# Optimization experiments

Measured on AMD Instinct MI355X. Metric: run time of the kernel, lower is better.

Reference implementation:

```python
import jax, jax.numpy as jnp
import numpy as np

C = 256      # embed_dim
GROUP = 2    # conv groups
K = 3        # kernel/pool size
K2 = K * K
OG = 8       # offset groups (hard-coded in Similarity_cal)
NEX = 3      # exemplars per image (out_conv expects group*3*4 channels)


def conv2d(x, w, b, pad):
    y = jax.lax.conv_general_dilated(x, w, (1, 1), [(pad, pad), (pad, pad)],
                                     dimension_numbers=("NCHW", "OIHW", "NCHW"))
    return y + b[None, :, None, None]


def ln_c(x, g, b, eps=1e-5):
    # LayerNorm over the channel axis of NCHW (torch permutes to NHWC, LN, permute back)
    mu = x.mean(axis=1, keepdims=True)
    var = ((x - mu) ** 2).mean(axis=1, keepdims=True)
    return (x - mu) / jnp.sqrt(var + eps) * g[None, :, None, None] + b[None, :, None, None]


def bilinear_gather(img, py, px):
    # img [Cg,H,W]; py,px [K2,H,W] -> samples [Cg,K2,H,W], zero outside borders
    Cg, H, W = img.shape
    y0f = jnp.floor(py); x0f = jnp.floor(px)
    wy = py - y0f; wx = px - x0f
    y0 = y0f.astype(jnp.int32); x0 = x0f.astype(jnp.int32)
    flat = img.reshape(Cg, H * W)

    def corner(yy, xx, w):
        valid = (yy >= 0) & (yy < H) & (xx >= 0) & (xx < W)
        idx = jnp.clip(yy, 0, H - 1) * W + jnp.clip(xx, 0, W - 1)
        v = jnp.take(flat, idx.reshape(-1), axis=1).reshape(Cg, K2, H, W)
        return v * (w * valid)[None]

    return (corner(y0, x0, (1 - wy) * (1 - wx)) + corner(y0, x0 + 1, (1 - wy) * wx)
            + corner(y0 + 1, x0, wy * (1 - wx)) + corner(y0 + 1, x0 + 1, wy * wx))


def deform_conv(x, offset, mask, weight, dilation):
    # x [C,H,W]; offset [2*OG*K2,H,W]; mask [OG*K2,H,W] (softmaxed); weight [NEX*GROUP, C//GROUP, K, K]
    Cc, H, W = x.shape
    pad = (K - 1) * dilation // 2
    off = offset.reshape(OG, K2, 2, H, W)  # (dy, dx) per offset-group / tap
    kk = jnp.arange(K, dtype=x.dtype)
    ky = jnp.repeat(kk, K) * dilation - pad  # [K2]
    kx = jnp.tile(kk, K) * dilation - pad
    ii = jnp.arange(H, dtype=x.dtype)
    jj = jnp.arange(W, dtype=x.dtype)
    py = ii[None, None, :, None] + ky[None, :, None, None] + off[:, :, 0]  # [OG,K2,H,W]
    px = jj[None, None, None, :] + kx[None, :, None, None] + off[:, :, 1]
    xg = x.reshape(OG, Cc // OG, H, W)
    samp = jax.vmap(bilinear_gather)(xg, py, px)              # [OG,Cg,K2,H,W]
    samp = samp * mask.reshape(OG, 1, K2, H, W)               # modulation
    samp = samp.reshape(GROUP, Cc // GROUP, K2, H, W)
    wR = weight.reshape(NEX * GROUP, Cc // GROUP, K2)
    gidx = jnp.arange(NEX * GROUP) // NEX                     # out-channel -> conv group
    return jnp.einsum("rck,rckhw->rhw", wR, samp[gidx])       # [NEX*GROUP,H,W]


def forward(querys_feat, supports_feat, in_w, in_b, ln_g, ln_b, out_w, out_b,
            offw1, offb1, mskw1, mskb1, offw2, offb2, mskw2, mskb2,
            offw4, offb4, mskw4, mskb4):
    B = querys_feat.shape[0]
    q = ln_c(conv2d(querys_feat, in_w, in_b, 0), ln_g, ln_b)                 # [B,C,H,W]
    s = supports_feat.reshape(B * NEX, C, K, K)
    s = ln_c(conv2d(s, in_w, in_b, 0), ln_g, ln_b).reshape(B, NEX, C, K, K)

    def offs(wo, bo, wm, bm):
        o = conv2d(q, wo, bo, (K - 1) // 2)
        m = jax.nn.softmax(conv2d(q, wm, bm, (K - 1) // 2), axis=1)  # softmax over all OG*K2 channels
        return o, m

    o1, m1 = offs(offw1, offb1, mskw1, mskb1)
    o2, m2 = offs(offw2, offb2, mskw2, mskb2)
    o4, m4 = offs(offw4, offb4, mskw4, mskb4)

    def per_sample(qi, si, o1i, m1i, o2i, m2i, o4i, m4i):
        w = si.reshape(NEX * GROUP, C // GROUP, K, K)         # dynamic per-exemplar kernels
        pooled = si.max(axis=(2, 3)).reshape(NEX * GROUP, C // GROUP)
        gidx = jnp.arange(NEX * GROUP) // NEX
        qg = qi.reshape(GROUP, C // GROUP, *qi.shape[1:])
        sim0 = jnp.einsum("rc,rchw->rhw", pooled, qg[gidx])   # grouped 1x1 conv branch
        d1 = deform_conv(qi, o1i, m1i, w, 1)
        d2 = deform_conv(qi, o2i, m2i, w, 2)
        d4 = deform_conv(qi, o4i, m4i, w, 4)
        return jnp.concatenate([sim0, d1, d2, d4], axis=0)    # [GROUP*3*4, H, W]

    sim = jax.vmap(per_sample)(q, s, o1, m1, o2, m2, o4, m4)
    return conv2d(sim, out_w, out_b, 0)                        # [B,C,H,W]


def setup_inputs() -> dict:
    key = jax.random.key(0)
    ks = jax.random.split(key, 20)
    B, H, W = 2, 96, 96
    inp = {
        "querys_feat": jax.random.normal(ks[0], (B, C, H, W), jnp.float32),
        "supports_feat": jax.random.normal(ks[1], (B, NEX, C, K, K), jnp.float32),
        "in_w": jax.random.normal(ks[2], (C, C, 1, 1), jnp.float32) / 16.0,
        "in_b": jax.random.normal(ks[3], (C,), jnp.float32) * 0.02,
        "ln_g": jnp.ones((C,), jnp.float32),
        "ln_b": jnp.zeros((C,), jnp.float32),
        "out_w": jax.random.normal(ks[4], (C, GROUP * 3 * 4, 1, 1), jnp.float32) * 0.2,
        "out_b": jax.random.normal(ks[5], (C,), jnp.float32) * 0.02,
    }
    i = 6
    for d in (1, 2, 4):
        inp[f"offw{d}"] = jax.random.normal(ks[i], (2 * OG * K2, C, K, K), jnp.float32) * 0.01; i += 1
        inp[f"offb{d}"] = jax.random.normal(ks[i], (2 * OG * K2,), jnp.float32) * 0.1; i += 1
        inp[f"mskw{d}"] = jax.random.normal(ks[i], (OG * K2, C, K, K), jnp.float32) * 0.02; i += 1
        inp[f"mskb{d}"] = jax.random.normal(ks[i], (OG * K2,), jnp.float32) * 0.1; i += 1
    return inp


def reference(querys_feat, supports_feat, in_w, in_b, ln_g, ln_b, out_w, out_b,
              offw1, offb1, mskw1, mskb1, offw2, offb2, mskw2, mskb2,
              offw4, offb4, mskw4, mskb4):
    return forward(querys_feat, supports_feat, in_w, in_b, ln_g, ln_b, out_w, out_b,
                   offw1, offb1, mskw1, mskb1, offw2, offb2, mskw2, mskb2,
                   offw4, offb4, mskw4, mskb4)
```

## Files before the change

kernel.cpp:

```cpp
#include <hip/hip_runtime.h>
#include <hip/hip_bf16.h>
#include <math.h>

#define HH 96
#define WWID 96
#define HW 9216
#define CC 256
#define BB 2
#define PROW 104
#define PCOL 128
#define PPX (PROW * PCOL)

typedef float f32x4 __attribute__((ext_vector_type(4)));
typedef _Float16 f16x8 __attribute__((ext_vector_type(8)));
typedef _Float16 h2v __attribute__((ext_vector_type(2)));

__device__ inline unsigned int pack2h(float a, float b) {
  unsigned short ua = __builtin_bit_cast(unsigned short, (_Float16)a);
  unsigned short ub = __builtin_bit_cast(unsigned short, (_Float16)b);
  return (unsigned int)ua | ((unsigned int)ub << 16);
}

#if defined(__has_builtin)
#if __has_builtin(__builtin_amdgcn_fdot2)
#define FDOT2(a, b, c) __builtin_amdgcn_fdot2((a), (b), (c), false)
#endif
#endif
#ifndef FDOT2
#define FDOT2(a, b, c) ((c) + (float)(a).x * (float)(b).x + (float)(a).y * (float)(b).y)
#endif

__device__ inline void gload_lds16(const void* g, void* l) {
  __builtin_amdgcn_global_load_lds(
      (const __attribute__((address_space(1))) void*)g,
      (__attribute__((address_space(3))) void*)l, 16, 0, 0);
}

__global__ void k_prep(const float* __restrict__ in_w, float* __restrict__ wT,
                       const float* __restrict__ ow1, const float* __restrict__ ob1,
                       const float* __restrict__ mw1, const float* __restrict__ mb1,
                       const float* __restrict__ ow2, const float* __restrict__ ob2,
                       const float* __restrict__ mw2, const float* __restrict__ mb2,
                       const float* __restrict__ ow4, const float* __restrict__ ob4,
                       const float* __restrict__ mw4, const float* __restrict__ mb4,
                       _Float16* __restrict__ Whf, float* __restrict__ Ball) {
  int bx = blockIdx.x;
  int t = threadIdx.x;
  if (bx < 256) {
    wT[bx * CC + t] = in_w[t * CC + bx];
    return;
  }
  int idx = (bx - 256) * 256 + t;
  if (idx >= 3 * 256 * 2304) return;
  int d = idx / (256 * 2304);
  int rem = idx - d * 256 * 2304;
  int co = rem / 2304;
  int k = rem - co * 2304;
  int j = k >> 8, ci = k & 255;
  const float* ow = d == 0 ? ow1 : (d == 1 ? ow2 : ow4);
  const float* mw = d == 0 ? mw1 : (d == 1 ? mw2 : mw4);
  float v = 0.f;
  if (co < 144) v = ow[co * 2304 + ci * 9 + j];
  else if (co < 216) v = mw[(co - 144) * 2304 + ci * 9 + j];
  Whf[idx] = (_Float16)v;
  if (idx < 768) {
    int dd = idx >> 8, cc = idx & 255;
    const float* obv = dd == 0 ? ob1 : (dd == 1 ? ob2 : ob4);
    const float* mbv = dd == 0 ? mb1 : (dd == 1 ? mb2 : mb4);
    float bv = 0.f;
    if (cc < 144) bv = obv[cc];
    else if (cc < 216) bv = mbv[cc - 144];
    Ball[idx] = bv;
  }
}

__global__ void k_conv1_ln_q(const float* __restrict__ qin, const float* __restrict__ wT,
                             const float* __restrict__ in_b, const float* __restrict__ ln_g,
                             const float* __restrict__ ln_b, const float* __restrict__ pooled,
                             _Float16* __restrict__ qpad, float* __restrict__ sim) {
  int bx = blockIdx.x;
  int b = bx / 288;
  int hw0 = (bx % 288) * 32;
  int t = threadIdx.x;
  int lane = t & 63;
  int wv_id = t >> 6;
  __shared__ float xs[32 * 260];
  const float* qb = qin + (size_t)b * CC * HW;
  #pragma unroll
  for (int i = 0; i < 32; ++i) {
    int idx = t + i * 256;
    int p = idx & 31;
    int k = idx >> 5;
    xs[p * 260 + k] = qb[k * HW + hw0 + p];
  }
  __syncthreads();
  float acc[8][4];
  #pragma unroll
  for (int p = 0; p < 8; ++p) { acc[p][0]=0.f; acc[p][1]=0.f; acc[p][2]=0.f; acc[p][3]=0.f; }
  const float4* wT4 = (const float4*)wT;
  int p0 = wv_id * 8;
  for (int k = 0; k < 256; k += 4) {
    float4 w0 = wT4[(k + 0) * 64 + lane];
    float4 w1 = wT4[(k + 1) * 64 + lane];
    float4 w2 = wT4[(k + 2) * 64 + lane];
    float4 w3 = wT4[(k + 3) * 64 + lane];
    #pragma unroll
    for (int p = 0; p < 8; ++p) {
      float4 xv = *(const float4*)&xs[(p0 + p) * 260 + k];
      acc[p][0] += w0.x * xv.x + w1.x * xv.y + w2.x * xv.z + w3.x * xv.w;
      acc[p][1] += w0.y * xv.x + w1.y * xv.y + w2.y * xv.z + w3.y * xv.w;
      acc[p][2] += w0.z * xv.x + w1.z * xv.y + w2.z * xv.z + w3.z * xv.w;
      acc[p][3] += w0.w * xv.x + w1.w * xv.y + w2.w * xv.z + w3.w * xv.w;
    }
  }
  float4 bb = ((const float4*)in_b)[lane];
  float4 g4 = ((const float4*)ln_g)[lane];
  float4 b4 = ((const float4*)ln_b)[lane];
  int lg = lane >> 5;
  int lc = lane & 31;
  const float4* pp = (const float4*)(pooled + (size_t)b * 768 + (lg * 3) * 128);
  float4 pr0 = pp[lc];
  float4 pr1 = pp[32 + lc];
  float4 pr2 = pp[64 + lc];
  #pragma unroll
  for (int p = 0; p < 8; ++p) {
    float y0 = acc[p][0] + bb.x, y1 = acc[p][1] + bb.y;
    float y2 = acc[p][2] + bb.z, y3 = acc[p][3] + bb.w;
    float s1 = y0 + y1 + y2 + y3;
    float s2 = y0*y0 + y1*y1 + y2*y2 + y3*y3;
    #pragma unroll
    for (int off = 32; off; off >>= 1) { s1 += __shfl_xor(s1, off); s2 += __shfl_xor(s2, off); }
    float mu = s1 * (1.f / 256.f);
    float rstd = rsqrtf(s2 * (1.f / 256.f) - mu * mu + 1e-5f);
    float4 o;
    o.x = (y0 - mu) * rstd * g4.x + b4.x;
    o.y = (y1 - mu) * rstd * g4.y + b4.y;
    o.z = (y2 - mu) * rstd * g4.z + b4.z;
    o.w = (y3 - mu) * rstd * g4.w + b4.w;
    int hw = hw0 + p0 + p;
    int hh = hw / 96, ww = hw - hh * 96;
    int ppx = (hh + 4) * PCOL + ww + 4;
    struct alignas(8) h4 { _Float16 h[4]; };
    h4 oh;
    oh.h[0] = (_Float16)o.x; oh.h[1] = (_Float16)o.y;
    oh.h[2] = (_Float16)o.z; oh.h[3] = (_Float16)o.w;
    *(h4*)(qpad + ((size_t)b * PPX + ppx) * CC + lane * 4) = oh;
    float r0 = pr0.x * o.x + pr0.y * o.y + pr0.z * o.z + pr0.w * o.w;
    float r1 = pr1.x * o.x + pr1.y * o.y + pr1.z * o.z + pr1.w * o.w;
    float r2 = pr2.x * o.x + pr2.y * o.y + pr2.z * o.z + pr2.w * o.w;
    #pragma unroll
    for (int off = 16; off; off >>= 1) {
      r0 += __shfl_xor(r0, off);
      r1 += __shfl_xor(r1, off);
      r2 += __shfl_xor(r2, off);
    }
    if (lc == 0) {
      size_t base = ((size_t)b * 24 + lg * 3) * HW + hw;
      sim[base] = r0;
      sim[base + HW] = r1;
      sim[base + 2 * HW] = r2;
    }
  }
}

__global__ void k_conv1_ln_s(const float* __restrict__ sup, const float* __restrict__ wT,
                             const float* __restrict__ in_b, const float* __restrict__ ln_g,
                             const float* __restrict__ ln_b, float* __restrict__ s_ln,
                             float* __restrict__ pooled) {
  int img = blockIdx.x;
  int t = threadIdx.x;
  int wv = t >> 6;
  int lane = t & 63;
  __shared__ float xs[2304];
  __shared__ float r1s[4][9], r2s[4][9];
  #pragma unroll
  for (int p = 0; p < 9; ++p) xs[t * 9 + p] = sup[(size_t)img * 2304 + t * 9 + p];
  __syncthreads();
  float acc[9];
  #pragma unroll
  for (int p = 0; p < 9; ++p) acc[p] = 0.f;
  for (int k = 0; k < 256; ++k) {
    float wv_ = wT[k * CC + t];
    #pragma unroll
    for (int p = 0; p < 9; ++p) acc[p] += wv_ * xs[k * 9 + p];
  }
  float bias = in_b[t];
  #pragma unroll
  for (int p = 0; p < 9; ++p) acc[p] += bias;
  #pragma unroll
  for (int p = 0; p < 9; ++p) {
    float s1 = acc[p];
    float s2 = acc[p] * acc[p];
    #pragma unroll
    for (int off = 32; off; off >>= 1) { s1 += __shfl_xor(s1, off); s2 += __shfl_xor(s2, off); }
    if (lane == 0) { r1s[wv][p] = s1; r2s[wv][p] = s2; }
  }
  __syncthreads();
  float g = ln_g[t], be = ln_b[t];
  float vals[9];
  #pragma unroll
  for (int p = 0; p < 9; ++p) {
    float s1 = r1s[0][p] + r1s[1][p] + r1s[2][p] + r1s[3][p];
    float s2 = r2s[0][p] + r2s[1][p] + r2s[2][p] + r2s[3][p];
    float mu = s1 * (1.f / 256.f);
    float var = s2 * (1.f / 256.f) - mu * mu;
    float rstd = rsqrtf(var + 1e-5f);
    vals[p] = (acc[p] - mu) * rstd * g + be;
  }
  #pragma unroll
  for (int p = 0; p < 9; ++p) s_ln[(size_t)img * 2304 + t * 9 + p] = vals[p];
  float mx = vals[0];
  #pragma unroll
  for (int p = 1; p < 9; ++p) mx = fmaxf(mx, vals[p]);
  int b = img / 3, e = img % 3;
  pooled[((size_t)b * 6 + e * 2 + (t >> 7)) * 128 + (t & 127)] = mx;
}


#define BAR() __builtin_amdgcn_s_barrier()
#define SCHEDB() __builtin_amdgcn_sched_barrier(0)
#define VMCNT(N) asm volatile("s_waitcnt vmcnt(" #N ")" ::: "memory")

#define MMA_ONE(M, N, S, QM, QN) \
  acc[(QM)*4+(M)][(QN)*2+(N)] = __builtin_amdgcn_mfma_f32_16x16x32_f16( \
      af[M][S], bf[(QN)*2+(N)][S], acc[(QM)*4+(M)][(QN)*2+(N)], 0, 0, 0);

#define MMA_Q(QM, QN) { \
  __builtin_amdgcn_s_setprio(1); \
  MMA_ONE(0,0,0,QM,QN) MMA_ONE(1,0,0,QM,QN) MMA_ONE(2,0,0,QM,QN) MMA_ONE(3,0,0,QM,QN) \
  MMA_ONE(0,1,0,QM,QN) MMA_ONE(1,1,0,QM,QN) MMA_ONE(2,1,0,QM,QN) MMA_ONE(3,1,0,QM,QN) \
  MMA_ONE(0,0,1,QM,QN) MMA_ONE(1,0,1,QM,QN) MMA_ONE(2,0,1,QM,QN) MMA_ONE(3,0,1,QM,QN) \
  MMA_ONE(0,1,1,QM,QN) MMA_ONE(1,1,1,QM,QN) MMA_ONE(2,1,1,QM,QN) MMA_ONE(3,1,1,QM,QN) \
  __builtin_amdgcn_s_setprio(0); }

#define LDA(BUF, QM) { \
  const char* p_ = smemB + (BUF) * 65536 + (wm * 128 + (QM) * 64 + l15) * 128; \
  af[0][0] = *(const f16x8*)(p_ + 0*2048 + rc0); af[0][1] = *(const f16x8*)(p_ + 0*2048 + rc1); \
  af[1][0] = *(const f16x8*)(p_ + 1*2048 + rc0); af[1][1] = *(const f16x8*)(p_ + 1*2048 + rc1); \
  af[2][0] = *(const f16x8*)(p_ + 2*2048 + rc0); af[2][1] = *(const f16x8*)(p_ + 2*2048 + rc1); \
  af[3][0] = *(const f16x8*)(p_ + 3*2048 + rc0); af[3][1] = *(const f16x8*)(p_ + 3*2048 + rc1); }

#define LDB(BUF, QN) { \
  const char* p_ = smemB + (BUF) * 65536 + 32768 + (wn * 64 + (QN) * 32 + l15) * 128; \
  bf[(QN)*2+0][0] = *(const f16x8*)(p_ + 0*2048 + rc0); bf[(QN)*2+0][1] = *(const f16x8*)(p_ + 0*2048 + rc1); \
  bf[(QN)*2+1][0] = *(const f16x8*)(p_ + 1*2048 + rc0); bf[(QN)*2+1][1] = *(const f16x8*)(p_ + 1*2048 + rc1); }

#define STAGEA(TILE, Q) { \
  gload_lds16(aBase + (size_t)((Q) * 64) * 2304 + (TILE) * 64, \
              smemB + ((TILE) & 1) * 65536 + (((Q) * 64 + wv * 8) * 128)); \
  gload_lds16(aBase + (size_t)(128 + (Q) * 64) * 2304 + (TILE) * 64, \
              smemB + ((TILE) & 1) * 65536 + ((128 + (Q) * 64 + wv * 8) * 128)); }

#define STAGEB(TILE, Q, PPX0, PPX1) { \
  int j_ = (TILE) >> 2; \
  int offp_ = (j_ / 3 - 1) * PCOL + (j_ % 3) - 1; \
  int cb_ = ((TILE) & 3) * 64; \
  int rs_ = (wv >> 2) * 64 + (Q) * 32 + (wv & 3) * 8; \
  gload_lds16(bBase + (size_t)((PPX0) + offp_) * CC + cb_, \
              smemB + ((TILE) & 1) * 65536 + 32768 + (rs_ * 128)); \
  gload_lds16(bBase + (size_t)((PPX1) + offp_) * CC + cb_, \
              smemB + ((TILE) & 1) * 65536 + 32768 + ((128 + rs_) * 128)); }

__global__ void __launch_bounds__(512) k_conv3_mfma8(
    const _Float16* __restrict__ qpad, const _Float16* __restrict__ Whf,
    const float* __restrict__ Ball, unsigned int* __restrict__ taprec) {
  int nb = blockIdx.x;
  int z = blockIdx.y;
  int d = z >> 1, b = z & 1;
  int t = threadIdx.x;
  int lane = t & 63, wv = t >> 6;
  int wm = wv >> 2, wn = wv & 3;
  int quad = lane >> 4, l15 = lane & 15;
  int l8 = lane >> 3, c7 = lane & 7;

  __shared__ _Float16 __attribute__((aligned(16))) smem[65536];
  char* smemB = (char*)smem;

  const _Float16* Wd = Whf + (size_t)d * 256 * 2304;
  const _Float16* qb = qpad + (size_t)b * PPX * CC;

  int scol = ((c7 ^ l8) << 3);
  int rc0 = ((quad ^ (l15 & 7)) << 4);
  int rc1 = (((4 | quad) ^ (l15 & 7)) << 4);

  const _Float16* aBase = Wd + (size_t)(wv * 8 + l8) * 2304 + scol;
  const _Float16* bBase = qb + scol;

  int ppx00, ppx01, ppx10, ppx11;
  {
    int rbase = (wv >> 2) * 64 + (wv & 3) * 8 + l8;
    int px, hh, ww;
    px = nb * 256 + rbase;             hh = px / 96; ww = px - hh * 96; ppx00 = (hh + 4) * PCOL + ww + 4;
    px = nb * 256 + 128 + rbase;       hh = px / 96; ww = px - hh * 96; ppx01 = (hh + 4) * PCOL + ww + 4;
    px = nb * 256 + 32 + rbase;        hh = px / 96; ww = px - hh * 96; ppx10 = (hh + 4) * PCOL + ww + 4;
    px = nb * 256 + 160 + rbase;       hh = px / 96; ww = px - hh * 96; ppx11 = (hh + 4) * PCOL + ww + 4;
  }

  f32x4 acc[8][4];
  #pragma unroll
  for (int i = 0; i < 8; ++i)
    #pragma unroll
    for (int j = 0; j < 4; ++j) acc[i][j] = (f32x4){0.f, 0.f, 0.f, 0.f};

  f16x8 af[4][2], bf[4][2];

  STAGEA(0, 0);
  STAGEB(0, 1, ppx10, ppx11);
  STAGEA(0, 1);
  STAGEB(0, 0, ppx00, ppx01);
  STAGEA(1, 0);
  STAGEB(1, 1, ppx10, ppx11);
  VMCNT(4);
  BAR();
  SCHEDB();

  #pragma unroll 1
  for (int ii = 0; ii < 17; ++ii) {
    int ta = 2 * ii + 1, tb = 2 * ii + 2, tc = 2 * ii + 3;
    LDA(0, 0) LDB(0, 0)
    STAGEA(ta, 1);
    BAR(); MMA_Q(0, 0); BAR();
    LDB(0, 1)
    STAGEB(ta, 0, ppx00, ppx01);
    BAR(); MMA_Q(0, 1); BAR();
    LDA(0, 1)
    STAGEA(tb, 0);
    BAR(); MMA_Q(1, 1); BAR();
    STAGEB(tb, 1, ppx10, ppx11);
    VMCNT(4);
    BAR(); SCHEDB(); MMA_Q(1, 0); BAR();
    LDA(1, 0) LDB(1, 0)
    STAGEA(tb, 1);
    BAR(); MMA_Q(0, 0); BAR();
    LDB(1, 1)
    STAGEB(tb, 0, ppx00, ppx01);
    BAR(); MMA_Q(0, 1); BAR();
    LDA(1, 1)
    STAGEA(tc, 0);
    BAR(); MMA_Q(1, 1); BAR();
    STAGEB(tc, 1, ppx10, ppx11);
    VMCNT(4);
    BAR(); SCHEDB(); MMA_Q(1, 0); BAR();
  }

  LDA(0, 0) LDB(0, 0)
  STAGEA(35, 1);
  BAR(); MMA_Q(0, 0); BAR();
  LDB(0, 1)
  STAGEB(35, 0, ppx00, ppx01);
  BAR(); MMA_Q(0, 1); BAR();
  LDA(0, 1)
  BAR(); MMA_Q(1, 1); BAR();
  VMCNT(0);
  BAR(); SCHEDB(); MMA_Q(1, 0); BAR();
  LDA(1, 0) LDB(1, 0)
  BAR(); MMA_Q(0, 0); BAR();
  LDB(1, 1)
  BAR(); MMA_Q(0, 1); BAR();
  LDA(1, 1)
  BAR(); MMA_Q(1, 1); BAR();
  MMA_Q(1, 0);

  BAR();
  float* cs = (float*)smemB;
  const float* Bd = Ball + d * 256;
  unsigned int* tzo = taprec + (size_t)z * 72 * HW * 3;
  int sub = t & 7;
  int pxq = t >> 3;
  int dil = 1 << d;

  #pragma unroll 1
  for (int H = 0; H < 2; ++H) {
    if ((wn >> 1) == H) {
      #pragma unroll
      for (int mi = 0; mi < 8; ++mi) {
        int c2 = wm * 128 + mi * 16 + quad * 4;
        if (c2 < 216) {
          float4 bq = *(const float4*)(Bd + c2);
          #pragma unroll
          for (int ni = 0; ni < 4; ++ni) {
            int pl = (wn & 1) * 64 + ni * 16 + l15;
            f32x4 v = acc[mi][ni];
            float* cp = &cs[pl * 225 + c2];
            cp[0] = v[0] + bq.x; cp[1] = v[1] + bq.y;
            cp[2] = v[2] + bq.z; cp[3] = v[3] + bq.w;
          }
        }
      }
    }
    BAR();
    #pragma unroll 1
    for (int p = 0; p < 2; ++p) {
      int pl = p * 64 + pxq;
      int px = nb * 256 + H * 128 + pl;
      const float* cr = &cs[pl * 225];
      float lg[9];
      float mx = -1e30f;
      #pragma unroll
      for (int j = 0; j < 9; ++j) {
        lg[j] = cr[144 + sub + 8 * j];
        mx = fmaxf(mx, lg[j]);
      }
      mx = fmaxf(mx, __shfl_xor(mx, 1));
      mx = fmaxf(mx, __shfl_xor(mx, 2));
      mx = fmaxf(mx, __shfl_xor(mx, 4));
      float s = 0.f;
      #pragma unroll
      for (int j = 0; j < 9; ++j) s += __expf(lg[j] - mx);
      s += __shfl_xor(s, 1);
      s += __shfl_xor(s, 2);
      s += __shfl_xor(s, 4);
      float rinv = 1.f / s;
      int h = px / WWID, w = px - h * WWID;
      int k = sub;
      #pragma unroll
      for (int j = 0; j < 9; ++j) {
        int tk = sub + 8 * j;
        float dy = cr[tk * 2 + 0];
        float dx = cr[tk * 2 + 1];
        float m = __expf(lg[j] - mx) * rinv;
        float py = (float)(h + (k / 3) * dil - dil) + dy;
        float pxx = (float)(w + (k % 3) * dil - dil) + dx;
        float y0f = floorf(py), x0f = floorf(pxx);
        int y0 = (int)y0f, x0 = (int)x0f;
        float wy = py - y0f, wx = pxx - x0f;
        bool vy0 = (unsigned)y0 < 96u, vy1 = (unsigned)(y0 + 1) < 96u;
        bool vx0 = (unsigned)x0 < 96u, vx1 = (unsigned)(x0 + 1) < 96u;
        float w00 = (vy0 && vx0) ? (1.f - wy) * (1.f - wx) * m : 0.f;
        float w01 = (vy0 && vx1) ? (1.f - wy) * wx * m : 0.f;
        float w10 = (vy1 && vx0) ? wy * (1.f - wx) * m : 0.f;
        float w11 = (vy1 && vx1) ? wy * wx * m : 0.f;
        int iy = min(max(y0 + 4, 0), 102);
        int ix = min(max(x0 + 4, 0), 126);
        unsigned int* r = tzo + ((size_t)tk * HW + px) * 3;
        r[0] = pack2h(w00, w01);
        r[1] = pack2h(w10, w11);
        r[2] = (unsigned int)(iy * PCOL + ix);
        k += 8; if (k >= 9) k -= 9;
      }
    }
    BAR();
  }
}

#define DO_P(U0, U1, IDX, P) { \
  h2v u0_ = __builtin_bit_cast(h2v, (U0)); \
  h2v u1_ = __builtin_bit_cast(h2v, (U1)); \
  const h2v* b0_ = qc + (size_t)(IDX) * 128; \
  h2v q00_ = b0_[0], q01_ = b0_[128]; \
  h2v q10_ = b0_[16384], q11_ = b0_[16384 + 128]; \
  h2v s_ = q00_ * (h2v){u0_.x, u0_.x} + q01_ * (h2v){u0_.y, u0_.y} \
         + q10_ * (h2v){u1_.x, u1_.x} + q11_ * (h2v){u1_.y, u1_.y}; \
  acc[P][0] = FDOT2(wr0, s_, acc[P][0]); \
  acc[P][1] = FDOT2(wr1, s_, acc[P][1]); \
  acc[P][2] = FDOT2(wr2, s_, acc[P][2]); }

__global__ void __launch_bounds__(256) k_deform(
    const _Float16* __restrict__ qpad, const unsigned int* __restrict__ taprec,
    const float* __restrict__ s_ln, float* __restrict__ sim) {
  int bid = blockIdx.x;
  int slab = bid & 7;
  int j = bid >> 3;
  int z = j / 72;
  int rem = j - z * 72;
  int yhalf = rem / 36;
  int segin = rem - yhalf * 36;
  int seg = slab * 36 + segin;
  int d_idx = z >> 1, b = z & 1;
  int t = threadIdx.x;
  int g = t >> 5, lane = t & 31;
  int half16 = lane >> 4, l16 = lane & 15;
  __shared__ _Float16 wh[9 * 384];
  __shared__ unsigned int __attribute__((aligned(16))) rlds[36 * 96];
  int px0 = seg * 32;
  int tkbase = yhalf * 36;
  const unsigned int* tz = taprec + (size_t)z * 72 * HW * 3;
  for (int i2 = t; i2 < 3456; i2 += 256) {
    int c = i2 / 9, k = i2 % 9;
    wh[k * 384 + c] = (_Float16)s_ln[(size_t)b * 6912 + yhalf * 3456 + i2];
  }
  for (int i2 = t; i2 < 3456; i2 += 256) {
    int tko = i2 / 96, dw = i2 - tko * 96;
    rlds[i2] = tz[((size_t)(tkbase + tko) * HW + px0) * 3 + dw];
  }
  __syncthreads();
  int pg = g * 4;
  int pxb = px0 + pg;
  const unsigned int* whd = (const unsigned int*)wh;
  const _Float16* qb = qpad + (size_t)b * PPX * CC;

  float acc[4][3];
  #pragma unroll
  for (int p = 0; p < 4; ++p)
    #pragma unroll
    for (int r = 0; r < 3; ++r) acc[p][r] = 0.f;

  #pragma unroll 1
  for (int ogp = 0; ogp < 2; ++ogp) {
    int og = yhalf * 4 + ogp * 2 + half16;
    int qch = og * 32 + l16 * 2;
    int wcol = qch - yhalf * 128;
    int tko = (ogp * 2 + half16) * 9;
    const h2v* qc = (const h2v*)(qb + qch);
    #pragma unroll 3
    for (int k = 0; k < 9; ++k) {
      const uint4* rr4 = (const uint4*)&rlds[(tko + k) * 96 + pg * 3];
      uint4 ra = rr4[0];
      uint4 rb = rr4[1];
      uint4 rc = rr4[2];
      h2v wr0 = __builtin_bit_cast(h2v, whd[(k * 384 + 0 + wcol) >> 1]);
      h2v wr1 = __builtin_bit_cast(h2v, whd[(k * 384 + 128 + wcol) >> 1]);
      h2v wr2 = __builtin_bit_cast(h2v, whd[(k * 384 + 256 + wcol) >> 1]);
      DO_P(ra.x, ra.y, ra.z, 0)
      DO_P(ra.w, rb.x, rb.y, 1)
      DO_P(rb.z, rb.w, rc.x, 2)
      DO_P(rc.y, rc.z, rc.w, 3)
    }
  }

  #pragma unroll
  for (int p = 0; p < 4; ++p) {
    #pragma unroll
    for (int r = 0; r < 3; ++r) {
      float v = acc[p][r];
      #pragma unroll
      for (int off = 16; off; off >>= 1) v += __shfl_down(v, off, 32);
      if (lane == 0)
        sim[((size_t)b * 24 + 6 + 6 * d_idx + yhalf * 3 + r) * HW + pxb + p] = v;
    }
  }
}

__global__ void k_outconv(const float* __restrict__ sim, const float* __restrict__ out_w,
                          const float* __restrict__ out_b, float* __restrict__ out) {
  int hw = blockIdx.x * 256 + threadIdx.x;
  int coq = blockIdx.y * 4;
  int b = blockIdx.z;
  const float* simb = sim + (size_t)b * 24 * HW;
  float a0 = out_b[coq + 0];
  float a1 = out_b[coq + 1];
  float a2 = out_b[coq + 2];
  float a3 = out_b[coq + 3];
  #pragma unroll
  for (int r = 0; r < 24; ++r) {
    float sv = simb[(size_t)r * HW + hw];
    a0 += out_w[(coq + 0) * 24 + r] * sv;
    a1 += out_w[(coq + 1) * 24 + r] * sv;
    a2 += out_w[(coq + 2) * 24 + r] * sv;
    a3 += out_w[(coq + 3) * 24 + r] * sv;
  }
  size_t base = ((size_t)b * CC + coq) * HW + hw;
  out[base] = a0;
  out[base + HW] = a1;
  out[base + 2 * HW] = a2;
  out[base + 3 * HW] = a3;
}

extern "C" void kernel_launch(void* const* d_in, const int* in_sizes, int n_in,
                              void* d_out, int out_size, void* d_ws, size_t ws_size,
                              hipStream_t stream) {
  const float* querys = (const float*)d_in[0];
  const float* sup    = (const float*)d_in[1];
  const float* in_w   = (const float*)d_in[2];
  const float* in_b   = (const float*)d_in[3];
  const float* ln_g   = (const float*)d_in[4];
  const float* ln_b   = (const float*)d_in[5];
  const float* out_w  = (const float*)d_in[6];
  const float* out_b  = (const float*)d_in[7];
  const float* ow1 = (const float*)d_in[8];
  const float* ob1 = (const float*)d_in[9];
  const float* mw1 = (const float*)d_in[10];
  const float* mb1 = (const float*)d_in[11];
  const float* ow2 = (const float*)d_in[12];
  const float* ob2 = (const float*)d_in[13];
  const float* mw2 = (const float*)d_in[14];
  const float* mb2 = (const float*)d_in[15];
  const float* ow4 = (const float*)d_in[16];
  const float* ob4 = (const float*)d_in[17];
  const float* mw4 = (const float*)d_in[18];
  const float* mb4 = (const float*)d_in[19];
  float* out = (float*)d_out;

  float* ws_f   = (float*)d_ws;
  float* wT     = ws_f;
  _Float16* Whf = (_Float16*)(wT + 65536);
  float* Ball   = (float*)(Whf + 3 * 256 * 2304);
  _Float16* qpad = (_Float16*)(Ball + 1024);
  float* s_ln   = (float*)(qpad + (size_t)BB * PPX * CC);
  float* pooled = s_ln + 13824;
  unsigned int* taprec = (unsigned int*)(pooled + 1536);
  float* sim    = (float*)(taprec + (size_t)6 * 72 * HW * 3);

  hipMemsetAsync(qpad, 0, (size_t)BB * PPX * CC * sizeof(_Float16), stream);
  k_prep<<<dim3(256 + 6912), dim3(256), 0, stream>>>(
      in_w, wT, ow1, ob1, mw1, mb1, ow2, ob2, mw2, mb2, ow4, ob4, mw4, mb4, Whf, Ball);
  k_conv1_ln_s<<<dim3(6), dim3(256), 0, stream>>>(sup, wT, in_b, ln_g, ln_b, s_ln, pooled);
  k_conv1_ln_q<<<dim3(576), dim3(256), 0, stream>>>(querys, wT, in_b, ln_g, ln_b, pooled, qpad, sim);
  k_conv3_mfma8<<<dim3(36, 6), dim3(512), 0, stream>>>(qpad, Whf, Ball, taprec);
  k_deform<<<dim3(3456), dim3(256), 0, stream>>>(qpad, taprec, s_ln, sim);
  k_outconv<<<dim3(36, 64, BB), dim3(256), 0, stream>>>(sim, out_w, out_b, out);
}
```

Measured before the change: 341.9 us.

## Widen deform gather to 4 channels per lane and pad tap LDS rows

The deformable sampling kernel now assigns each lane 4 fp16 channels instead of 2, so the two offset-group iterations fold into a single loop. Each bilinear corner fetch becomes one 8-byte load, with the blend done in packed half4 and fed to paired fdot2 accumulations. The LDS tap-record rows are padded from 96 to 100 words to change the bank mapping. The weight-prep kernel also handles 4 elements per thread with a quarter of the blocks, which trims launch overhead but adds register pressure and per-element index arithmetic.

```diff
diff --git a/kernel.cpp b/kernel.cpp
--- a/kernel.cpp
+++ b/kernel.cpp
@@ -14,6 +14,7 @@
 typedef float f32x4 __attribute__((ext_vector_type(4)));
 typedef _Float16 f16x8 __attribute__((ext_vector_type(8)));
 typedef _Float16 h2v __attribute__((ext_vector_type(2)));
+typedef _Float16 h4v __attribute__((ext_vector_type(4)));
 
 __device__ inline unsigned int pack2h(float a, float b) {
   unsigned short ua = __builtin_bit_cast(unsigned short, (_Float16)a);
@@ -50,27 +51,31 @@
     wT[bx * CC + t] = in_w[t * CC + bx];
     return;
   }
-  int idx = (bx - 256) * 256 + t;
-  if (idx >= 3 * 256 * 2304) return;
-  int d = idx / (256 * 2304);
-  int rem = idx - d * 256 * 2304;
-  int co = rem / 2304;
-  int k = rem - co * 2304;
-  int j = k >> 8, ci = k & 255;
-  const float* ow = d == 0 ? ow1 : (d == 1 ? ow2 : ow4);
-  const float* mw = d == 0 ? mw1 : (d == 1 ? mw2 : mw4);
-  float v = 0.f;
-  if (co < 144) v = ow[co * 2304 + ci * 9 + j];
-  else if (co < 216) v = mw[(co - 144) * 2304 + ci * 9 + j];
-  Whf[idx] = (_Float16)v;
-  if (idx < 768) {
-    int dd = idx >> 8, cc = idx & 255;
-    const float* obv = dd == 0 ? ob1 : (dd == 1 ? ob2 : ob4);
-    const float* mbv = dd == 0 ? mb1 : (dd == 1 ? mb2 : mb4);
-    float bv = 0.f;
-    if (cc < 144) bv = obv[cc];
-    else if (cc < 216) bv = mbv[cc - 144];
-    Ball[idx] = bv;
+  int idx0 = (bx - 256) * 1024 + t * 4;
+  if (idx0 >= 3 * 256 * 2304) return;
+  #pragma unroll
+  for (int u = 0; u < 4; ++u) {
+    int idx = idx0 + u;
+    int d = idx / (256 * 2304);
+    int rem = idx - d * 256 * 2304;
+    int co = rem / 2304;
+    int k = rem - co * 2304;
+    int j = k >> 8, ci = k & 255;
+    const float* ow = d == 0 ? ow1 : (d == 1 ? ow2 : ow4);
+    const float* mw = d == 0 ? mw1 : (d == 1 ? mw2 : mw4);
+    float v = 0.f;
+    if (co < 144) v = ow[co * 2304 + ci * 9 + j];
+    else if (co < 216) v = mw[(co - 144) * 2304 + ci * 9 + j];
+    Whf[idx] = (_Float16)v;
+    if (idx < 768) {
+      int dd = idx >> 8, cc = idx & 255;
+      const float* obv = dd == 0 ? ob1 : (dd == 1 ? ob2 : ob4);
+      const float* mbv = dd == 0 ? mb1 : (dd == 1 ? mb2 : mb4);
+      float bv = 0.f;
+      if (cc < 144) bv = obv[cc];
+      else if (cc < 216) bv = mbv[cc - 144];
+      Ball[idx] = bv;
+    }
   }
 }
 
@@ -443,17 +448,25 @@
   }
 }
 
-#define DO_P(U0, U1, IDX, P) { \
+#define DO_P4(U0, U1, IDX, P) { \
   h2v u0_ = __builtin_bit_cast(h2v, (U0)); \
   h2v u1_ = __builtin_bit_cast(h2v, (U1)); \
-  const h2v* b0_ = qc + (size_t)(IDX) * 128; \
-  h2v q00_ = b0_[0], q01_ = b0_[128]; \
-  h2v q10_ = b0_[16384], q11_ = b0_[16384 + 128]; \
-  h2v s_ = q00_ * (h2v){u0_.x, u0_.x} + q01_ * (h2v){u0_.y, u0_.y} \
-         + q10_ * (h2v){u1_.x, u1_.x} + q11_ * (h2v){u1_.y, u1_.y}; \
-  acc[P][0] = FDOT2(wr0, s_, acc[P][0]); \
-  acc[P][1] = FDOT2(wr1, s_, acc[P][1]); \
-  acc[P][2] = FDOT2(wr2, s_, acc[P][2]); }
+  const h4v* b0_ = qc + (size_t)(IDX) * 64; \
+  h4v q00_ = b0_[0], q01_ = b0_[64]; \
+  h4v q10_ = b0_[8192], q11_ = b0_[8192 + 64]; \
+  h4v s_ = q00_ * (h4v){u0_.x, u0_.x, u0_.x, u0_.x} \
+         + q01_ * (h4v){u0_.y, u0_.y, u0_.y, u0_.y} \
+         + q10_ * (h4v){u1_.x, u1_.x, u1_.x, u1_.x} \
+         + q11_ * (h4v){u1_.y, u1_.y, u1_.y, u1_.y}; \
+  uint2 su_ = __builtin_bit_cast(uint2, s_); \
+  h2v slo_ = __builtin_bit_cast(h2v, su_.x); \
+  h2v shi_ = __builtin_bit_cast(h2v, su_.y); \
+  acc[P][0] = FDOT2(wr0lo, slo_, acc[P][0]); \
+  acc[P][0] = FDOT2(wr0hi, shi_, acc[P][0]); \
+  acc[P][1] = FDOT2(wr1lo, slo_, acc[P][1]); \
+  acc[P][1] = FDOT2(wr1hi, shi_, acc[P][1]); \
+  acc[P][2] = FDOT2(wr2lo, slo_, acc[P][2]); \
+  acc[P][2] = FDOT2(wr2hi, shi_, acc[P][2]); }
 
 __global__ void __launch_bounds__(256) k_deform(
     const _Float16* __restrict__ qpad, const unsigned int* __restrict__ taprec,
@@ -469,9 +482,10 @@
   int d_idx = z >> 1, b = z & 1;
   int t = threadIdx.x;
   int g = t >> 5, lane = t & 31;
-  int half16 = lane >> 4, l16 = lane & 15;
-  __shared__ _Float16 wh[9 * 384];
-  __shared__ unsigned int __attribute__((aligned(16))) rlds[36 * 96];
+  int og_in = lane >> 3;
+  int l8c = lane & 7;
+  __shared__ _Float16 __attribute__((aligned(16))) wh[9 * 384];
+  __shared__ unsigned int __attribute__((aligned(16))) rlds[36 * 100];
   int px0 = seg * 32;
   int tkbase = yhalf * 36;
   const unsigned int* tz = taprec + (size_t)z * 72 * HW * 3;
@@ -481,41 +495,45 @@
   }
   for (int i2 = t; i2 < 3456; i2 += 256) {
     int tko = i2 / 96, dw = i2 - tko * 96;
-    rlds[i2] = tz[((size_t)(tkbase + tko) * HW + px0) * 3 + dw];
+    rlds[tko * 100 + dw] = tz[((size_t)(tkbase + tko) * HW + px0) * 3 + dw];
   }
   __syncthreads();
   int pg = g * 4;
   int pxb = px0 + pg;
-  const unsigned int* whd = (const unsigned int*)wh;
+  const h4v* whp = (const h4v*)wh;
   const _Float16* qb = qpad + (size_t)b * PPX * CC;
 
+  int wcol = og_in * 32 + l8c * 4;
+  int qch = yhalf * 128 + wcol;
+  int tko0 = og_in * 9;
+  const h4v* qc = (const h4v*)(qb + qch);
+
   float acc[4][3];
   #pragma unroll
   for (int p = 0; p < 4; ++p)
     #pragma unroll
     for (int r = 0; r < 3; ++r) acc[p][r] = 0.f;
 
-  #pragma unroll 1
-  for (int ogp = 0; ogp < 2; ++ogp) {
-    int og = yhalf * 4 + ogp * 2 + half16;
-    int qch = og * 32 + l16 * 2;
-    int wcol = qch - yhalf * 128;
-    int tko = (ogp * 2 + half16) * 9;
-    const h2v* qc = (const h2v*)(qb + qch);
-    #pragma unroll 3
-    for (int k = 0; k < 9; ++k) {
-      const uint4* rr4 = (const uint4*)&rlds[(tko + k) * 96 + pg * 3];
-      uint4 ra = rr4[0];
-      uint4 rb = rr4[1];
-      uint4 rc = rr4[2];
-      h2v wr0 = __builtin_bit_cast(h2v, whd[(k * 384 + 0 + wcol) >> 1]);
-      h2v wr1 = __builtin_bit_cast(h2v, whd[(k * 384 + 128 + wcol) >> 1]);
-      h2v wr2 = __builtin_bit_cast(h2v, whd[(k * 384 + 256 + wcol) >> 1]);
-      DO_P(ra.x, ra.y, ra.z, 0)
-      DO_P(ra.w, rb.x, rb.y, 1)
-      DO_P(rb.z, rb.w, rc.x, 2)
-      DO_P(rc.y, rc.z, rc.w, 3)
-    }
+  #pragma unroll 3
+  for (int k = 0; k < 9; ++k) {
+    const uint4* rr4 = (const uint4*)&rlds[(tko0 + k) * 100 + pg * 3];
+    uint4 ra = rr4[0];
+    uint4 rb = rr4[1];
+    uint4 rc = rr4[2];
+    int wbase = k * 96 + (wcol >> 2);
+    h4v w0 = whp[wbase];
+    h4v w1 = whp[wbase + 32];
+    h4v w2 = whp[wbase + 64];
+    uint2 w0u = __builtin_bit_cast(uint2, w0);
+    uint2 w1u = __builtin_bit_cast(uint2, w1);
+    uint2 w2u = __builtin_bit_cast(uint2, w2);
+    h2v wr0lo = __builtin_bit_cast(h2v, w0u.x), wr0hi = __builtin_bit_cast(h2v, w0u.y);
+    h2v wr1lo = __builtin_bit_cast(h2v, w1u.x), wr1hi = __builtin_bit_cast(h2v, w1u.y);
+    h2v wr2lo = __builtin_bit_cast(h2v, w2u.x), wr2hi = __builtin_bit_cast(h2v, w2u.y);
+    DO_P4(ra.x, ra.y, ra.z, 0)
+    DO_P4(ra.w, rb.x, rb.y, 1)
+    DO_P4(rb.z, rb.w, rc.x, 2)
+    DO_P4(rc.y, rc.z, rc.w, 3)
   }
 
   #pragma unroll
@@ -592,7 +610,7 @@
   float* sim    = (float*)(taprec + (size_t)6 * 72 * HW * 3);
 
   hipMemsetAsync(qpad, 0, (size_t)BB * PPX * CC * sizeof(_Float16), stream);
-  k_prep<<<dim3(256 + 6912), dim3(256), 0, stream>>>(
+  k_prep<<<dim3(256 + 1728), dim3(256), 0, stream>>>(
       in_w, wT, ow1, ob1, mw1, mb1, ow2, ob2, mw2, mb2, ow4, ob4, mw4, mb4, Whf, Ball);
   k_conv1_ln_s<<<dim3(6), dim3(256), 0, stream>>>(sup, wT, in_b, ln_g, ln_b, s_ln, pooled);
   k_conv1_ln_q<<<dim3(576), dim3(256), 0, stream>>>(querys, wT, in_b, ln_g, ln_b, pooled, qpad, sim);
```

Measured after the change: 354.4 us. +3.6%, slower.
